# Kernel optimization log

Hardware: AMD Instinct MI355X
Metric: run time of the kernel (lower is better)

## Reference

```python
import jax, jax.numpy as jnp
import numpy as np

N = 100000   # nodes
E = 1600000  # edges (avg degree 16)
DIN = 64
DOUT = 64
EPS = 1e-12  # F.normalize eps


def setup_inputs() -> dict:
    key = jax.random.key(0)
    ks = jax.random.split(key, 10)
    x = jax.random.normal(ks[0], (N, DIN), dtype=jnp.float32)
    edge_index = jax.random.randint(ks[1], (2, E), 0, N, dtype=jnp.int32)
    edge_feature = jax.random.normal(ks[2], (E, 8), dtype=jnp.float32)
    s_in = 1.0 / np.sqrt(DIN)
    s_out = 1.0 / np.sqrt(DOUT)
    # layer 1: SAGEConv(DIN, DOUT, aggr='sum'): lin_l (bias) on aggregate, lin_r (no bias) on root
    W1l = jax.random.uniform(ks[3], (DOUT, DIN), jnp.float32, -s_in, s_in)
    b1l = jax.random.uniform(ks[4], (DOUT,), jnp.float32, -s_in, s_in)
    W1r = jax.random.uniform(ks[5], (DOUT, DIN), jnp.float32, -s_in, s_in)
    # layer 2: SAGEConv(DOUT, DOUT, aggr='sum')
    W2l = jax.random.uniform(ks[6], (DOUT, DOUT), jnp.float32, -s_out, s_out)
    b2l = jax.random.uniform(ks[7], (DOUT,), jnp.float32, -s_out, s_out)
    W2r = jax.random.uniform(ks[8], (DOUT, DOUT), jnp.float32, -s_out, s_out)
    return {"x": x, "edge_index": edge_index, "edge_feature": edge_feature,
            "W1l": W1l, "b1l": b1l, "W1r": W1r,
            "W2l": W2l, "b2l": b2l, "W2r": W2r}


def _sage_conv(x, src, dst, Wl, bl, Wr):
    # sum-aggregate neighbor messages x[src] at destination nodes
    agg = jax.ops.segment_sum(x[src], dst, num_segments=N)  # [N, d]
    return agg @ Wl.T + bl + x @ Wr.T


def reference(x, edge_index, edge_feature, W1l, b1l, W1r, W2l, b2l, W2r):
    # edge_feature is accepted by the original forward but unused
    src, dst = edge_index[0], edge_index[1]
    h = _sage_conv(x, src, dst, W1l, b1l, W1r)
    h = jax.nn.relu(h)
    nrm = jnp.linalg.norm(h, axis=-1, keepdims=True)
    h = h / jnp.maximum(nrm, EPS)  # F.normalize(dim=-1)
    # dropout is identity in eval mode
    out = _sage_conv(h, src, dst, W2l, b2l, W2r)
    return out
```

## Files before the change

kernel.cpp:

```cpp
#include <hip/hip_runtime.h>

#define NNODES 100000
#define NEDGES 1600000
#define D 64
#define EPSN 1e-12f
#define NBUK ((NNODES + 255) >> 8)
#define EPB 2048
#define LCAP 28
#define BUKCAP 4608

typedef __attribute__((ext_vector_type(8))) short short8v;
typedef __attribute__((ext_vector_type(4))) float f32x4;
typedef unsigned short ushort_t;

__device__ __forceinline__ unsigned f2bf(float f) {
    unsigned u = __float_as_uint(f);
    u = (u + 0x7FFFu + ((u >> 16) & 1u)) >> 16;
    return u;
}

__global__ __launch_bounds__(256) void cvt_bf16_kernel(
    const float* __restrict__ xin, ushort_t* __restrict__ xb)
{
    const int idx = blockIdx.x * 256 + threadIdx.x;
    if ((size_t)idx * 4 >= (size_t)NNODES * D) return;
    const float4 v = *reinterpret_cast<const float4*>(&xin[(size_t)idx * 4]);
    uint2 o;
    o.x = f2bf(v.x) | (f2bf(v.y) << 16);
    o.y = f2bf(v.z) | (f2bf(v.w) << 16);
    *reinterpret_cast<uint2*>(&xb[(size_t)idx * 4]) = o;
}

__global__ __launch_bounds__(256) void bin_scatter_kernel(
    const int* __restrict__ src,
    const int* __restrict__ dst,
    int* __restrict__ bukcnt,
    int* __restrict__ ebuf)
{
    __shared__ int lcnt[NBUK];
    __shared__ int bins[NBUK * LCAP];
    const int t = threadIdx.x;
    for (int i = t; i < NBUK; i += 256) lcnt[i] = 0;
    __syncthreads();

    const long long e0 = (long long)blockIdx.x * EPB + (long long)t * 8;
    if (e0 + 8 <= NEDGES) {
        const int4 sa = *reinterpret_cast<const int4*>(&src[e0]);
        const int4 sb = *reinterpret_cast<const int4*>(&src[e0 + 4]);
        const int4 da = *reinterpret_cast<const int4*>(&dst[e0]);
        const int4 db = *reinterpret_cast<const int4*>(&dst[e0 + 4]);
        const int dd[8] = {da.x, da.y, da.z, da.w, db.x, db.y, db.z, db.w};
        const int ss[8] = {sa.x, sa.y, sa.z, sa.w, sb.x, sb.y, sb.z, sb.w};
        #pragma unroll
        for (int i = 0; i < 8; ++i) {
            const int b = dd[i] >> 8;
            const int p = atomicAdd(&lcnt[b], 1);
            if (p < LCAP) bins[b * LCAP + p] = (ss[i] << 8) | (dd[i] & 255);
        }
    } else {
        for (long long e = e0; e < NEDGES; ++e) {
            const int d = dst[e];
            const int b = d >> 8;
            const int p = atomicAdd(&lcnt[b], 1);
            if (p < LCAP) bins[b * LCAP + p] = (src[e] << 8) | (d & 255);
        }
    }
    __syncthreads();

    for (int b = t; b < NBUK; b += 256) {
        const int cnt = min(lcnt[b], LCAP);
        if (cnt == 0) continue;
        const int base = atomicAdd(&bukcnt[b], cnt);
        for (int i = 0; i < cnt; ++i) {
            const int p = base + i;
            if (p < BUKCAP) ebuf[(size_t)b * BUKCAP + p] = bins[b * LCAP + i];
        }
    }
}

__global__ void bukscan_kernel(const int* __restrict__ bukcnt,
                               int* __restrict__ bukstart) {
    __shared__ int s[512];
    const int t = threadIdx.x;
    const int v = (t < NBUK) ? min(bukcnt[t], BUKCAP) : 0;
    int val = v;
    s[t] = val;
    __syncthreads();
    for (int off = 1; off < 512; off <<= 1) {
        int add = (t >= off) ? s[t - off] : 0;
        __syncthreads();
        val += add;
        s[t] = val;
        __syncthreads();
    }
    if (t < NBUK) bukstart[t] = val - v;
}

__global__ __launch_bounds__(256) void bucket_place_kernel(
    const int* __restrict__ bukcnt,
    const int* __restrict__ bukstart,
    const int* __restrict__ ebuf,
    int* __restrict__ rowptr,
    int* __restrict__ ssrc)
{
    __shared__ int lcnt[256];
    __shared__ int lcur[256];
    __shared__ int stmp[256];
    const int b = blockIdx.x;
    const int t = threadIdx.x;
    lcnt[t] = 0;
    lcur[t] = 0;
    __syncthreads();

    const int cnt  = min(bukcnt[b], BUKCAP);
    const int base = bukstart[b];
    const int* eb  = ebuf + (size_t)b * BUKCAP;

    for (int i = t; i < cnt; i += 256) atomicAdd(&lcnt[eb[i] & 255], 1);
    __syncthreads();

    const int v = lcnt[t];
    int val = v;
    stmp[t] = val;
    __syncthreads();
    for (int off = 1; off < 256; off <<= 1) {
        int add = (t >= off) ? stmp[t - off] : 0;
        __syncthreads();
        val += add;
        stmp[t] = val;
        __syncthreads();
    }
    const int myoff = val - v;
    __syncthreads();
    lcnt[t] = myoff;
    const int node = b * 256 + t;
    if (node < NNODES) rowptr[node] = base + myoff;
    if (b == NBUK - 1 && t == 0) rowptr[NNODES] = base + cnt;
    __syncthreads();

    for (int i = t; i < cnt; i += 256) {
        const int pv = eb[i];
        const int d = pv & 255;
        const int p = atomicAdd(&lcur[d], 1);
        ssrc[base + lcnt[d] + p] = pv >> 8;
    }
}

__global__ __launch_bounds__(256) void gather_bf16_kernel(
    const ushort_t* __restrict__ featb,
    const int* __restrict__ rowptr,
    const int* __restrict__ ssrc,
    ushort_t* __restrict__ aggb)
{
    const int tid = threadIdx.x;
    const int quarter = tid >> 4;
    const int f = tid & 15;
    const int node = blockIdx.x * 16 + quarter;
    if (node >= NNODES) return;

    const int beg = rowptr[node];
    const int end = rowptr[node + 1];
    const ushort_t* fb = featb + (size_t)f * 4;

    float ax = 0.f, ay = 0.f, az = 0.f, aw = 0.f;
    int j = beg;
    for (; j + 4 <= end; j += 4) {
        const int s0 = ssrc[j + 0];
        const int s1 = ssrc[j + 1];
        const int s2 = ssrc[j + 2];
        const int s3 = ssrc[j + 3];
        const uint2 v0 = *reinterpret_cast<const uint2*>(&fb[(size_t)s0 * D]);
        const uint2 v1 = *reinterpret_cast<const uint2*>(&fb[(size_t)s1 * D]);
        const uint2 v2 = *reinterpret_cast<const uint2*>(&fb[(size_t)s2 * D]);
        const uint2 v3 = *reinterpret_cast<const uint2*>(&fb[(size_t)s3 * D]);
        ax += __uint_as_float(v0.x << 16) + __uint_as_float(v1.x << 16)
            + __uint_as_float(v2.x << 16) + __uint_as_float(v3.x << 16);
        ay += __uint_as_float(v0.x & 0xFFFF0000u) + __uint_as_float(v1.x & 0xFFFF0000u)
            + __uint_as_float(v2.x & 0xFFFF0000u) + __uint_as_float(v3.x & 0xFFFF0000u);
        az += __uint_as_float(v0.y << 16) + __uint_as_float(v1.y << 16)
            + __uint_as_float(v2.y << 16) + __uint_as_float(v3.y << 16);
        aw += __uint_as_float(v0.y & 0xFFFF0000u) + __uint_as_float(v1.y & 0xFFFF0000u)
            + __uint_as_float(v2.y & 0xFFFF0000u) + __uint_as_float(v3.y & 0xFFFF0000u);
    }
    for (; j < end; ++j) {
        const uint2 v = *reinterpret_cast<const uint2*>(&fb[(size_t)ssrc[j] * D]);
        ax += __uint_as_float(v.x << 16);
        ay += __uint_as_float(v.x & 0xFFFF0000u);
        az += __uint_as_float(v.y << 16);
        aw += __uint_as_float(v.y & 0xFFFF0000u);
    }
    uint2 o;
    o.x = f2bf(ax) | (f2bf(ay) << 16);
    o.y = f2bf(az) | (f2bf(aw) << 16);
    *reinterpret_cast<uint2*>(&aggb[(size_t)node * D + f * 4]) = o;
}

__global__ void wprep_kernel(const float* __restrict__ W1l,
                             const float* __restrict__ W1r,
                             const float* __restrict__ W2l,
                             const float* __restrict__ W2r,
                             ushort_t* __restrict__ wfrag)
{
    const int idx = blockIdx.x * 256 + threadIdx.x;
    if (idx >= 16384) return;
    const int layer = idx >> 13;
    const int f     = (idx >> 9) & 15;
    const int lane  = (idx >> 3) & 63;
    const int b     = idx & 7;
    const int jt = f >> 2, kt = f & 3;
    const int o = jt * 16 + (lane & 15);
    const int k = kt * 32 + (lane >> 4) * 8 + b;
    const float* Wl = layer ? W2l : W1l;
    const float* Wr = layer ? W2r : W1r;
    const float v = (k < 64) ? Wl[o * 64 + k] : Wr[o * 64 + (k - 64)];
    wfrag[idx] = (ushort_t)f2bf(v);
}

#define LB(i) const short8v B##i = \
    *reinterpret_cast<const short8v*>(&wfragL[((i) * 64 + lane) * 8]);

template <bool RELU_NORM, bool BF16_OUT>
__global__ __launch_bounds__(256) void transform_mfma_kernel(
    const ushort_t* __restrict__ aggb,
    const ushort_t* __restrict__ xinb,
    const ushort_t* __restrict__ wfragL,
    const float* __restrict__ bl,
    float* __restrict__ outf,
    ushort_t* __restrict__ outb)
{
    const int tid  = threadIdx.x;
    const int w    = tid >> 6;
    const int lane = tid & 63;
    const int m    = lane & 15;
    const int kg   = lane >> 4;

    LB(0)  LB(1)  LB(2)  LB(3)  LB(4)  LB(5)  LB(6)  LB(7)
    LB(8)  LB(9)  LB(10) LB(11) LB(12) LB(13) LB(14) LB(15)

    const float bias0 = bl[m];
    const float bias1 = bl[16 + m];
    const float bias2 = bl[32 + m];
    const float bias3 = bl[48 + m];

    const int ngroups = NNODES / 16;
    for (int g = blockIdx.x * 4 + w; g < ngroups; g += gridDim.x * 4) {
        const size_t rb = (size_t)(g * 16 + m) * D;
        const short8v A0 = *reinterpret_cast<const short8v*>(&aggb[rb + kg * 8]);
        const short8v A1 = *reinterpret_cast<const short8v*>(&aggb[rb + 32 + kg * 8]);
        const short8v A2 = *reinterpret_cast<const short8v*>(&xinb[rb + kg * 8]);
        const short8v A3 = *reinterpret_cast<const short8v*>(&xinb[rb + 32 + kg * 8]);

        f32x4 acc0 = {0.f, 0.f, 0.f, 0.f};
        f32x4 acc1 = acc0, acc2 = acc0, acc3 = acc0;
        acc0 = __builtin_amdgcn_mfma_f32_16x16x32_bf16(A0, B0,  acc0, 0, 0, 0);
        acc0 = __builtin_amdgcn_mfma_f32_16x16x32_bf16(A1, B1,  acc0, 0, 0, 0);
        acc0 = __builtin_amdgcn_mfma_f32_16x16x32_bf16(A2, B2,  acc0, 0, 0, 0);
        acc0 = __builtin_amdgcn_mfma_f32_16x16x32_bf16(A3, B3,  acc0, 0, 0, 0);
        acc1 = __builtin_amdgcn_mfma_f32_16x16x32_bf16(A0, B4,  acc1, 0, 0, 0);
        acc1 = __builtin_amdgcn_mfma_f32_16x16x32_bf16(A1, B5,  acc1, 0, 0, 0);
        acc1 = __builtin_amdgcn_mfma_f32_16x16x32_bf16(A2, B6,  acc1, 0, 0, 0);
        acc1 = __builtin_amdgcn_mfma_f32_16x16x32_bf16(A3, B7,  acc1, 0, 0, 0);
        acc2 = __builtin_amdgcn_mfma_f32_16x16x32_bf16(A0, B8,  acc2, 0, 0, 0);
        acc2 = __builtin_amdgcn_mfma_f32_16x16x32_bf16(A1, B9,  acc2, 0, 0, 0);
        acc2 = __builtin_amdgcn_mfma_f32_16x16x32_bf16(A2, B10, acc2, 0, 0, 0);
        acc2 = __builtin_amdgcn_mfma_f32_16x16x32_bf16(A3, B11, acc2, 0, 0, 0);
        acc3 = __builtin_amdgcn_mfma_f32_16x16x32_bf16(A0, B12, acc3, 0, 0, 0);
        acc3 = __builtin_amdgcn_mfma_f32_16x16x32_bf16(A1, B13, acc3, 0, 0, 0);
        acc3 = __builtin_amdgcn_mfma_f32_16x16x32_bf16(A2, B14, acc3, 0, 0, 0);
        acc3 = __builtin_amdgcn_mfma_f32_16x16x32_bf16(A3, B15, acc3, 0, 0, 0);

        acc0 += bias0; acc1 += bias1; acc2 += bias2; acc3 += bias3;

        if (RELU_NORM) {
            #pragma unroll
            for (int r = 0; r < 4; ++r) {
                acc0[r] = fmaxf(acc0[r], 0.f);
                acc1[r] = fmaxf(acc1[r], 0.f);
                acc2[r] = fmaxf(acc2[r], 0.f);
                acc3[r] = fmaxf(acc3[r], 0.f);
            }
            float s0 = acc0[0]*acc0[0] + acc1[0]*acc1[0] + acc2[0]*acc2[0] + acc3[0]*acc3[0];
            float s1 = acc0[1]*acc0[1] + acc1[1]*acc1[1] + acc2[1]*acc2[1] + acc3[1]*acc3[1];
            float s2 = acc0[2]*acc0[2] + acc1[2]*acc1[2] + acc2[2]*acc2[2] + acc3[2]*acc3[2];
            float s3 = acc0[3]*acc0[3] + acc1[3]*acc1[3] + acc2[3]*acc2[3] + acc3[3]*acc3[3];
            #pragma unroll
            for (int mm = 1; mm < 16; mm <<= 1) {
                s0 += __shfl_xor(s0, mm, 64);
                s1 += __shfl_xor(s1, mm, 64);
                s2 += __shfl_xor(s2, mm, 64);
                s3 += __shfl_xor(s3, mm, 64);
            }
            const float i0 = 1.f / fmaxf(sqrtf(s0), EPSN);
            const float i1 = 1.f / fmaxf(sqrtf(s1), EPSN);
            const float i2 = 1.f / fmaxf(sqrtf(s2), EPSN);
            const float i3 = 1.f / fmaxf(sqrtf(s3), EPSN);
            acc0[0] *= i0; acc1[0] *= i0; acc2[0] *= i0; acc3[0] *= i0;
            acc0[1] *= i1; acc1[1] *= i1; acc2[1] *= i1; acc3[1] *= i1;
            acc0[2] *= i2; acc1[2] *= i2; acc2[2] *= i2; acc3[2] *= i2;
            acc0[3] *= i3; acc1[3] *= i3; acc2[3] *= i3; acc3[3] *= i3;
        }

        #pragma unroll
        for (int r = 0; r < 4; ++r) {
            const size_t row = (size_t)(g * 16 + kg * 4 + r) * D + m;
            if (BF16_OUT) {
                outb[row]      = (ushort_t)f2bf(acc0[r]);
                outb[row + 16] = (ushort_t)f2bf(acc1[r]);
                outb[row + 32] = (ushort_t)f2bf(acc2[r]);
                outb[row + 48] = (ushort_t)f2bf(acc3[r]);
            } else {
                outf[row]      = acc0[r];
                outf[row + 16] = acc1[r];
                outf[row + 32] = acc2[r];
                outf[row + 48] = acc3[r];
            }
        }
    }
}

extern "C" void kernel_launch(void* const* d_in, const int* in_sizes, int n_in,
                              void* d_out, int out_size, void* d_ws, size_t ws_size,
                              hipStream_t stream) {
    const float* x   = (const float*)d_in[0];
    const int* eidx  = (const int*)d_in[1];
    const float* W1l = (const float*)d_in[3];
    const float* b1l = (const float*)d_in[4];
    const float* W1r = (const float*)d_in[5];
    const float* W2l = (const float*)d_in[6];
    const float* b2l = (const float*)d_in[7];
    const float* W2r = (const float*)d_in[8];
    float* out = (float*)d_out;

    const int* src = eidx;
    const int* dst = eidx + NEDGES;

    char* ws = (char*)d_ws;
    int* bukcnt   = (int*)ws;  ws += ((size_t)NBUK * 4 + 15) / 16 * 16;
    int* bukstart = (int*)ws;  ws += ((size_t)NBUK * 4 + 15) / 16 * 16;
    int* rowptr   = (int*)ws;  ws += ((size_t)(NNODES + 1) * 4 + 15) / 16 * 16;
    int* ssrc     = (int*)ws;  ws += ((size_t)NEDGES * 4 + 15) / 16 * 16;
    ushort_t* wfrag = (ushort_t*)ws;  ws += ((size_t)16384 * 2 + 15) / 16 * 16;
    ushort_t* xb  = (ushort_t*)ws;    ws += (size_t)NNODES * D * 2;
    ushort_t* hb  = (ushort_t*)ws;    ws += (size_t)NNODES * D * 2;
    ushort_t* aggb = (ushort_t*)ws;   ws += (size_t)NNODES * D * 2;
    int* ebuf = (int*)aggb;

    dim3 blk(256);
    dim3 bgrid((NEDGES + EPB - 1) / EPB);
    dim3 cgrid(((NNODES * D / 4) + 255) / 256);
    dim3 ggrid((NNODES + 15) / 16);
    dim3 tgrid(1024);

    hipMemsetAsync(bukcnt, 0, (size_t)NBUK * 4, stream);
    cvt_bf16_kernel<<<cgrid, blk, 0, stream>>>(x, xb);
    wprep_kernel<<<64, blk, 0, stream>>>(W1l, W1r, W2l, W2r, wfrag);
    bin_scatter_kernel<<<bgrid, blk, 0, stream>>>(src, dst, bukcnt, ebuf);
    bukscan_kernel<<<1, 512, 0, stream>>>(bukcnt, bukstart);
    bucket_place_kernel<<<NBUK, blk, 0, stream>>>(bukcnt, bukstart, ebuf,
                                                  rowptr, ssrc);

    gather_bf16_kernel<<<ggrid, blk, 0, stream>>>(xb, rowptr, ssrc, aggb);
    transform_mfma_kernel<true, true><<<tgrid, blk, 0, stream>>>(
        aggb, xb, wfrag, b1l, nullptr, hb);

    gather_bf16_kernel<<<ggrid, blk, 0, stream>>>(hb, rowptr, ssrc, aggb);
    transform_mfma_kernel<false, false><<<tgrid, blk, 0, stream>>>(
        aggb, hb, wfrag + 8192, b2l, out, nullptr);
}
```

Measured before the change: 187.9 us.

## Split bf16 features into four planar slices and gather each slice separately

Node features are stored as four planes of 16 bf16 columns each, and each gather becomes four passes that each touch a 3.2 MB plane. The aim is to let each plane's random-access working set fit in L2/LLC so neighbour gathers hit cache more often. The costs are four times as many index reads and kernel launches, 32-byte row reads instead of 128-byte ones, and scattered 2-byte stores in the planar output of the transform.

```diff
diff --git a/kernel.cpp b/kernel.cpp
--- a/kernel.cpp
+++ b/kernel.cpp
@@ -8,10 +8,12 @@
 #define EPB 2048
 #define LCAP 28
 #define BUKCAP 4608
+#define PL ((size_t)NNODES * 16)
 
 typedef __attribute__((ext_vector_type(8))) short short8v;
 typedef __attribute__((ext_vector_type(4))) float f32x4;
 typedef unsigned short ushort_t;
+typedef unsigned int uint_t;
 
 __device__ __forceinline__ unsigned f2bf(float f) {
     unsigned u = __float_as_uint(f);
@@ -19,16 +21,22 @@
     return u;
 }
 
-__global__ __launch_bounds__(256) void cvt_bf16_kernel(
-    const float* __restrict__ xin, ushort_t* __restrict__ xb)
+__global__ __launch_bounds__(256) void cvt_planar_kernel(
+    const float* __restrict__ xin, ushort_t* __restrict__ xbP)
 {
     const int idx = blockIdx.x * 256 + threadIdx.x;
-    if ((size_t)idx * 4 >= (size_t)NNODES * D) return;
-    const float4 v = *reinterpret_cast<const float4*>(&xin[(size_t)idx * 4]);
-    uint2 o;
-    o.x = f2bf(v.x) | (f2bf(v.y) << 16);
-    o.y = f2bf(v.z) | (f2bf(v.w) << 16);
-    *reinterpret_cast<uint2*>(&xb[(size_t)idx * 4]) = o;
+    if (idx >= NNODES * 8) return;
+    const int node = idx >> 3;
+    const int oct  = idx & 7;
+    const float4 a = *reinterpret_cast<const float4*>(&xin[(size_t)node * D + oct * 8]);
+    const float4 b = *reinterpret_cast<const float4*>(&xin[(size_t)node * D + oct * 8 + 4]);
+    uint4 o;
+    o.x = f2bf(a.x) | (f2bf(a.y) << 16);
+    o.y = f2bf(a.z) | (f2bf(a.w) << 16);
+    o.z = f2bf(b.x) | (f2bf(b.y) << 16);
+    o.w = f2bf(b.z) | (f2bf(b.w) << 16);
+    ushort_t* dst = xbP + (size_t)(oct >> 1) * PL + (size_t)node * 16 + (oct & 1) * 8;
+    *reinterpret_cast<uint4*>(dst) = o;
 }
 
 __global__ __launch_bounds__(256) void bin_scatter_kernel(
@@ -146,53 +154,45 @@
     }
 }
 
-__global__ __launch_bounds__(256) void gather_bf16_kernel(
-    const ushort_t* __restrict__ featb,
+__global__ __launch_bounds__(256) void gather_pass_kernel(
+    const ushort_t* __restrict__ featP,
     const int* __restrict__ rowptr,
     const int* __restrict__ ssrc,
-    ushort_t* __restrict__ aggb)
-{
-    const int tid = threadIdx.x;
-    const int quarter = tid >> 4;
-    const int f = tid & 15;
-    const int node = blockIdx.x * 16 + quarter;
+    ushort_t* __restrict__ aggP)
+{
+    const int tid  = threadIdx.x;
+    const int grp  = tid >> 3;
+    const int l    = tid & 7;
+    const int node = blockIdx.x * 32 + grp;
     if (node >= NNODES) return;
 
     const int beg = rowptr[node];
     const int end = rowptr[node + 1];
-    const ushort_t* fb = featb + (size_t)f * 4;
-
-    float ax = 0.f, ay = 0.f, az = 0.f, aw = 0.f;
+    const ushort_t* fb = featP + l * 2;
+
+    float ax = 0.f, ay = 0.f;
     int j = beg;
     for (; j + 4 <= end; j += 4) {
         const int s0 = ssrc[j + 0];
         const int s1 = ssrc[j + 1];
         const int s2 = ssrc[j + 2];
         const int s3 = ssrc[j + 3];
-        const uint2 v0 = *reinterpret_cast<const uint2*>(&fb[(size_t)s0 * D]);
-        const uint2 v1 = *reinterpret_cast<const uint2*>(&fb[(size_t)s1 * D]);
-        const uint2 v2 = *reinterpret_cast<const uint2*>(&fb[(size_t)s2 * D]);
-        const uint2 v3 = *reinterpret_cast<const uint2*>(&fb[(size_t)s3 * D]);
-        ax += __uint_as_float(v0.x << 16) + __uint_as_float(v1.x << 16)
-            + __uint_as_float(v2.x << 16) + __uint_as_float(v3.x << 16);
-        ay += __uint_as_float(v0.x & 0xFFFF0000u) + __uint_as_float(v1.x & 0xFFFF0000u)
-            + __uint_as_float(v2.x & 0xFFFF0000u) + __uint_as_float(v3.x & 0xFFFF0000u);
-        az += __uint_as_float(v0.y << 16) + __uint_as_float(v1.y << 16)
-            + __uint_as_float(v2.y << 16) + __uint_as_float(v3.y << 16);
-        aw += __uint_as_float(v0.y & 0xFFFF0000u) + __uint_as_float(v1.y & 0xFFFF0000u)
-            + __uint_as_float(v2.y & 0xFFFF0000u) + __uint_as_float(v3.y & 0xFFFF0000u);
+        const uint_t v0 = *reinterpret_cast<const uint_t*>(&fb[(size_t)s0 * 16]);
+        const uint_t v1 = *reinterpret_cast<const uint_t*>(&fb[(size_t)s1 * 16]);
+        const uint_t v2 = *reinterpret_cast<const uint_t*>(&fb[(size_t)s2 * 16]);
+        const uint_t v3 = *reinterpret_cast<const uint_t*>(&fb[(size_t)s3 * 16]);
+        ax += __uint_as_float(v0 << 16) + __uint_as_float(v1 << 16)
+            + __uint_as_float(v2 << 16) + __uint_as_float(v3 << 16);
+        ay += __uint_as_float(v0 & 0xFFFF0000u) + __uint_as_float(v1 & 0xFFFF0000u)
+            + __uint_as_float(v2 & 0xFFFF0000u) + __uint_as_float(v3 & 0xFFFF0000u);
     }
     for (; j < end; ++j) {
-        const uint2 v = *reinterpret_cast<const uint2*>(&fb[(size_t)ssrc[j] * D]);
-        ax += __uint_as_float(v.x << 16);
-        ay += __uint_as_float(v.x & 0xFFFF0000u);
-        az += __uint_as_float(v.y << 16);
-        aw += __uint_as_float(v.y & 0xFFFF0000u);
-    }
-    uint2 o;
-    o.x = f2bf(ax) | (f2bf(ay) << 16);
-    o.y = f2bf(az) | (f2bf(aw) << 16);
-    *reinterpret_cast<uint2*>(&aggb[(size_t)node * D + f * 4]) = o;
+        const uint_t v = *reinterpret_cast<const uint_t*>(&fb[(size_t)ssrc[j] * 16]);
+        ax += __uint_as_float(v << 16);
+        ay += __uint_as_float(v & 0xFFFF0000u);
+    }
+    *reinterpret_cast<uint_t*>(&aggP[(size_t)node * 16 + l * 2]) =
+        f2bf(ax) | (f2bf(ay) << 16);
 }
 
 __global__ void wprep_kernel(const float* __restrict__ W1l,
@@ -221,12 +221,12 @@
 
 template <bool RELU_NORM, bool BF16_OUT>
 __global__ __launch_bounds__(256) void transform_mfma_kernel(
-    const ushort_t* __restrict__ aggb,
-    const ushort_t* __restrict__ xinb,
+    const ushort_t* __restrict__ aggP,
+    const ushort_t* __restrict__ xinP,
     const ushort_t* __restrict__ wfragL,
     const float* __restrict__ bl,
     float* __restrict__ outf,
-    ushort_t* __restrict__ outb)
+    ushort_t* __restrict__ outbP)
 {
     const int tid  = threadIdx.x;
     const int w    = tid >> 6;
@@ -242,13 +242,15 @@
     const float bias2 = bl[32 + m];
     const float bias3 = bl[48 + m];
 
+    const size_t poff = (size_t)(kg >> 1) * PL + (size_t)(kg & 1) * 8;
+
     const int ngroups = NNODES / 16;
     for (int g = blockIdx.x * 4 + w; g < ngroups; g += gridDim.x * 4) {
-        const size_t rb = (size_t)(g * 16 + m) * D;
-        const short8v A0 = *reinterpret_cast<const short8v*>(&aggb[rb + kg * 8]);
-        const short8v A1 = *reinterpret_cast<const short8v*>(&aggb[rb + 32 + kg * 8]);
-        const short8v A2 = *reinterpret_cast<const short8v*>(&xinb[rb + kg * 8]);
-        const short8v A3 = *reinterpret_cast<const short8v*>(&xinb[rb + 32 + kg * 8]);
+        const size_t row16 = (size_t)(g * 16 + m) * 16;
+        const short8v A0 = *reinterpret_cast<const short8v*>(&aggP[poff + row16]);
+        const short8v A1 = *reinterpret_cast<const short8v*>(&aggP[poff + 2 * PL + row16]);
+        const short8v A2 = *reinterpret_cast<const short8v*>(&xinP[poff + row16]);
+        const short8v A3 = *reinterpret_cast<const short8v*>(&xinP[poff + 2 * PL + row16]);
 
         f32x4 acc0 = {0.f, 0.f, 0.f, 0.f};
         f32x4 acc1 = acc0, acc2 = acc0, acc3 = acc0;
@@ -302,13 +304,15 @@
 
         #pragma unroll
         for (int r = 0; r < 4; ++r) {
-            const size_t row = (size_t)(g * 16 + kg * 4 + r) * D + m;
+            const int nrow = g * 16 + kg * 4 + r;
             if (BF16_OUT) {
-                outb[row]      = (ushort_t)f2bf(acc0[r]);
-                outb[row + 16] = (ushort_t)f2bf(acc1[r]);
-                outb[row + 32] = (ushort_t)f2bf(acc2[r]);
-                outb[row + 48] = (ushort_t)f2bf(acc3[r]);
+                const size_t rb16 = (size_t)nrow * 16 + m;
+                outbP[rb16]          = (ushort_t)f2bf(acc0[r]);
+                outbP[PL + rb16]     = (ushort_t)f2bf(acc1[r]);
+                outbP[2 * PL + rb16] = (ushort_t)f2bf(acc2[r]);
+                outbP[3 * PL + rb16] = (ushort_t)f2bf(acc3[r]);
             } else {
+                const size_t row = (size_t)nrow * D + m;
                 outf[row]      = acc0[r];
                 outf[row + 16] = acc1[r];
                 outf[row + 32] = acc2[r];
@@ -340,30 +344,34 @@
     int* rowptr   = (int*)ws;  ws += ((size_t)(NNODES + 1) * 4 + 15) / 16 * 16;
     int* ssrc     = (int*)ws;  ws += ((size_t)NEDGES * 4 + 15) / 16 * 16;
     ushort_t* wfrag = (ushort_t*)ws;  ws += ((size_t)16384 * 2 + 15) / 16 * 16;
-    ushort_t* xb  = (ushort_t*)ws;    ws += (size_t)NNODES * D * 2;
-    ushort_t* hb  = (ushort_t*)ws;    ws += (size_t)NNODES * D * 2;
-    ushort_t* aggb = (ushort_t*)ws;   ws += (size_t)NNODES * D * 2;
-    int* ebuf = (int*)aggb;
+    ushort_t* xbP  = (ushort_t*)ws;   ws += PL * 4 * 2;
+    ushort_t* hbP  = (ushort_t*)ws;   ws += PL * 4 * 2;
+    ushort_t* aggP = (ushort_t*)ws;   ws += PL * 4 * 2;
+    int* ebuf = (int*)aggP;
 
     dim3 blk(256);
     dim3 bgrid((NEDGES + EPB - 1) / EPB);
-    dim3 cgrid(((NNODES * D / 4) + 255) / 256);
-    dim3 ggrid((NNODES + 15) / 16);
+    dim3 cgrid((NNODES * 8 + 255) / 256);
+    dim3 pgrid((NNODES + 31) / 32);
     dim3 tgrid(1024);
 
     hipMemsetAsync(bukcnt, 0, (size_t)NBUK * 4, stream);
-    cvt_bf16_kernel<<<cgrid, blk, 0, stream>>>(x, xb);
+    cvt_planar_kernel<<<cgrid, blk, 0, stream>>>(x, xbP);
     wprep_kernel<<<64, blk, 0, stream>>>(W1l, W1r, W2l, W2r, wfrag);
     bin_scatter_kernel<<<bgrid, blk, 0, stream>>>(src, dst, bukcnt, ebuf);
     bukscan_kernel<<<1, 512, 0, stream>>>(bukcnt, bukstart);
     bucket_place_kernel<<<NBUK, blk, 0, stream>>>(bukcnt, bukstart, ebuf,
                                                   rowptr, ssrc);
 
-    gather_bf16_kernel<<<ggrid, blk, 0, stream>>>(xb, rowptr, ssrc, aggb);
+    for (int p = 0; p < 4; ++p)
+        gather_pass_kernel<<<pgrid, blk, 0, stream>>>(
+            xbP + (size_t)p * PL, rowptr, ssrc, aggP + (size_t)p * PL);
     transform_mfma_kernel<true, true><<<tgrid, blk, 0, stream>>>(
-        aggb, xb, wfrag, b1l, nullptr, hb);
-
-    gather_bf16_kernel<<<ggrid, blk, 0, stream>>>(hb, rowptr, ssrc, aggb);
+        aggP, xbP, wfrag, b1l, nullptr, hbP);
+
+    for (int p = 0; p < 4; ++p)
+        gather_pass_kernel<<<pgrid, blk, 0, stream>>>(
+            hbP + (size_t)p * PL, rowptr, ssrc, aggP + (size_t)p * PL);
     transform_mfma_kernel<false, false><<<tgrid, blk, 0, stream>>>(
-        aggb, hb, wfrag + 8192, b2l, out, nullptr);
-}
+        aggP, hbP, wfrag + 8192, b2l, out, nullptr);
+}
```

Result: slower. 232.7 us (+23.8%).

## Fuse neighbor gather with MFMA transform per 16-node block

Applied to the files above, without the earlier changes.

Merges the gather kernel and the MFMA transform kernel into one kernel per layer. Each 16-node block aggregates neighbor rows into shared memory, loads the root features, and each wave computes one 16-column output slice with MFMA, adding a cross-wave shared-memory reduction for the L2 normalization. This removes the intermediate aggregate buffer round trip through global memory and two launches. In exchange each wave now reloads its weight fragments per block, adds __syncthreads barriers, and ebuf gets its own workspace region because it can no longer alias the removed aggregate buffer.

```diff
diff --git a/kernel.cpp b/kernel.cpp
--- a/kernel.cpp
+++ b/kernel.cpp
@@ -146,17 +146,57 @@
     }
 }
 
-__global__ __launch_bounds__(256) void gather_bf16_kernel(
+__global__ void wprep_kernel(const float* __restrict__ W1l,
+                             const float* __restrict__ W1r,
+                             const float* __restrict__ W2l,
+                             const float* __restrict__ W2r,
+                             ushort_t* __restrict__ wfrag)
+{
+    const int idx = blockIdx.x * 256 + threadIdx.x;
+    if (idx >= 16384) return;
+    const int layer = idx >> 13;
+    const int f     = (idx >> 9) & 15;
+    const int lane  = (idx >> 3) & 63;
+    const int b     = idx & 7;
+    const int jt = f >> 2, kt = f & 3;
+    const int o = jt * 16 + (lane & 15);
+    const int k = kt * 32 + (lane >> 4) * 8 + b;
+    const float* Wl = layer ? W2l : W1l;
+    const float* Wr = layer ? W2r : W1r;
+    const float v = (k < 64) ? Wl[o * 64 + k] : Wr[o * 64 + (k - 64)];
+    wfrag[idx] = (ushort_t)f2bf(v);
+}
+
+template <bool RELU_NORM, bool BF16_OUT>
+__global__ __launch_bounds__(256) void sage_gather_mfma_kernel(
     const ushort_t* __restrict__ featb,
     const int* __restrict__ rowptr,
     const int* __restrict__ ssrc,
-    ushort_t* __restrict__ aggb)
-{
+    const ushort_t* __restrict__ wfragL,
+    const float* __restrict__ bl,
+    float* __restrict__ outf,
+    ushort_t* __restrict__ outb)
+{
+    __shared__ ushort_t at[16][72];
+    __shared__ ushort_t xt[16][72];
+    __shared__ float ssq[4][16];
+
     const int tid = threadIdx.x;
     const int quarter = tid >> 4;
     const int f = tid & 15;
-    const int node = blockIdx.x * 16 + quarter;
-    if (node >= NNODES) return;
+    const int node0 = blockIdx.x * 16;
+    const int node = node0 + quarter;
+
+    const int w    = tid >> 6;
+    const int lane = tid & 63;
+    const int m    = lane & 15;
+    const int kg   = lane >> 4;
+
+    const short8v Bw0 = *reinterpret_cast<const short8v*>(&wfragL[((w * 4 + 0) * 64 + lane) * 8]);
+    const short8v Bw1 = *reinterpret_cast<const short8v*>(&wfragL[((w * 4 + 1) * 64 + lane) * 8]);
+    const short8v Bw2 = *reinterpret_cast<const short8v*>(&wfragL[((w * 4 + 2) * 64 + lane) * 8]);
+    const short8v Bw3 = *reinterpret_cast<const short8v*>(&wfragL[((w * 4 + 3) * 64 + lane) * 8]);
+    const float bias = bl[w * 16 + m];
 
     const int beg = rowptr[node];
     const int end = rowptr[node + 1];
@@ -189,132 +229,61 @@
         az += __uint_as_float(v.y << 16);
         aw += __uint_as_float(v.y & 0xFFFF0000u);
     }
-    uint2 o;
-    o.x = f2bf(ax) | (f2bf(ay) << 16);
-    o.y = f2bf(az) | (f2bf(aw) << 16);
-    *reinterpret_cast<uint2*>(&aggb[(size_t)node * D + f * 4]) = o;
-}
-
-__global__ void wprep_kernel(const float* __restrict__ W1l,
-                             const float* __restrict__ W1r,
-                             const float* __restrict__ W2l,
-                             const float* __restrict__ W2r,
-                             ushort_t* __restrict__ wfrag)
-{
-    const int idx = blockIdx.x * 256 + threadIdx.x;
-    if (idx >= 16384) return;
-    const int layer = idx >> 13;
-    const int f     = (idx >> 9) & 15;
-    const int lane  = (idx >> 3) & 63;
-    const int b     = idx & 7;
-    const int jt = f >> 2, kt = f & 3;
-    const int o = jt * 16 + (lane & 15);
-    const int k = kt * 32 + (lane >> 4) * 8 + b;
-    const float* Wl = layer ? W2l : W1l;
-    const float* Wr = layer ? W2r : W1r;
-    const float v = (k < 64) ? Wl[o * 64 + k] : Wr[o * 64 + (k - 64)];
-    wfrag[idx] = (ushort_t)f2bf(v);
-}
-
-#define LB(i) const short8v B##i = \
-    *reinterpret_cast<const short8v*>(&wfragL[((i) * 64 + lane) * 8]);
-
-template <bool RELU_NORM, bool BF16_OUT>
-__global__ __launch_bounds__(256) void transform_mfma_kernel(
-    const ushort_t* __restrict__ aggb,
-    const ushort_t* __restrict__ xinb,
-    const ushort_t* __restrict__ wfragL,
-    const float* __restrict__ bl,
-    float* __restrict__ outf,
-    ushort_t* __restrict__ outb)
-{
-    const int tid  = threadIdx.x;
-    const int w    = tid >> 6;
-    const int lane = tid & 63;
-    const int m    = lane & 15;
-    const int kg   = lane >> 4;
-
-    LB(0)  LB(1)  LB(2)  LB(3)  LB(4)  LB(5)  LB(6)  LB(7)
-    LB(8)  LB(9)  LB(10) LB(11) LB(12) LB(13) LB(14) LB(15)
-
-    const float bias0 = bl[m];
-    const float bias1 = bl[16 + m];
-    const float bias2 = bl[32 + m];
-    const float bias3 = bl[48 + m];
-
-    const int ngroups = NNODES / 16;
-    for (int g = blockIdx.x * 4 + w; g < ngroups; g += gridDim.x * 4) {
-        const size_t rb = (size_t)(g * 16 + m) * D;
-        const short8v A0 = *reinterpret_cast<const short8v*>(&aggb[rb + kg * 8]);
-        const short8v A1 = *reinterpret_cast<const short8v*>(&aggb[rb + 32 + kg * 8]);
-        const short8v A2 = *reinterpret_cast<const short8v*>(&xinb[rb + kg * 8]);
-        const short8v A3 = *reinterpret_cast<const short8v*>(&xinb[rb + 32 + kg * 8]);
-
-        f32x4 acc0 = {0.f, 0.f, 0.f, 0.f};
-        f32x4 acc1 = acc0, acc2 = acc0, acc3 = acc0;
-        acc0 = __builtin_amdgcn_mfma_f32_16x16x32_bf16(A0, B0,  acc0, 0, 0, 0);
-        acc0 = __builtin_amdgcn_mfma_f32_16x16x32_bf16(A1, B1,  acc0, 0, 0, 0);
-        acc0 = __builtin_amdgcn_mfma_f32_16x16x32_bf16(A2, B2,  acc0, 0, 0, 0);
-        acc0 = __builtin_amdgcn_mfma_f32_16x16x32_bf16(A3, B3,  acc0, 0, 0, 0);
-        acc1 = __builtin_amdgcn_mfma_f32_16x16x32_bf16(A0, B4,  acc1, 0, 0, 0);
-        acc1 = __builtin_amdgcn_mfma_f32_16x16x32_bf16(A1, B5,  acc1, 0, 0, 0);
-        acc1 = __builtin_amdgcn_mfma_f32_16x16x32_bf16(A2, B6,  acc1, 0, 0, 0);
-        acc1 = __builtin_amdgcn_mfma_f32_16x16x32_bf16(A3, B7,  acc1, 0, 0, 0);
-        acc2 = __builtin_amdgcn_mfma_f32_16x16x32_bf16(A0, B8,  acc2, 0, 0, 0);
-        acc2 = __builtin_amdgcn_mfma_f32_16x16x32_bf16(A1, B9,  acc2, 0, 0, 0);
-        acc2 = __builtin_amdgcn_mfma_f32_16x16x32_bf16(A2, B10, acc2, 0, 0, 0);
-        acc2 = __builtin_amdgcn_mfma_f32_16x16x32_bf16(A3, B11, acc2, 0, 0, 0);
-        acc3 = __builtin_amdgcn_mfma_f32_16x16x32_bf16(A0, B12, acc3, 0, 0, 0);
-        acc3 = __builtin_amdgcn_mfma_f32_16x16x32_bf16(A1, B13, acc3, 0, 0, 0);
-        acc3 = __builtin_amdgcn_mfma_f32_16x16x32_bf16(A2, B14, acc3, 0, 0, 0);
-        acc3 = __builtin_amdgcn_mfma_f32_16x16x32_bf16(A3, B15, acc3, 0, 0, 0);
-
-        acc0 += bias0; acc1 += bias1; acc2 += bias2; acc3 += bias3;
-
-        if (RELU_NORM) {
-            #pragma unroll
-            for (int r = 0; r < 4; ++r) {
-                acc0[r] = fmaxf(acc0[r], 0.f);
-                acc1[r] = fmaxf(acc1[r], 0.f);
-                acc2[r] = fmaxf(acc2[r], 0.f);
-                acc3[r] = fmaxf(acc3[r], 0.f);
-            }
-            float s0 = acc0[0]*acc0[0] + acc1[0]*acc1[0] + acc2[0]*acc2[0] + acc3[0]*acc3[0];
-            float s1 = acc0[1]*acc0[1] + acc1[1]*acc1[1] + acc2[1]*acc2[1] + acc3[1]*acc3[1];
-            float s2 = acc0[2]*acc0[2] + acc1[2]*acc1[2] + acc2[2]*acc2[2] + acc3[2]*acc3[2];
-            float s3 = acc0[3]*acc0[3] + acc1[3]*acc1[3] + acc2[3]*acc2[3] + acc3[3]*acc3[3];
-            #pragma unroll
-            for (int mm = 1; mm < 16; mm <<= 1) {
-                s0 += __shfl_xor(s0, mm, 64);
-                s1 += __shfl_xor(s1, mm, 64);
-                s2 += __shfl_xor(s2, mm, 64);
-                s3 += __shfl_xor(s3, mm, 64);
-            }
-            const float i0 = 1.f / fmaxf(sqrtf(s0), EPSN);
-            const float i1 = 1.f / fmaxf(sqrtf(s1), EPSN);
-            const float i2 = 1.f / fmaxf(sqrtf(s2), EPSN);
-            const float i3 = 1.f / fmaxf(sqrtf(s3), EPSN);
-            acc0[0] *= i0; acc1[0] *= i0; acc2[0] *= i0; acc3[0] *= i0;
-            acc0[1] *= i1; acc1[1] *= i1; acc2[1] *= i1; acc3[1] *= i1;
-            acc0[2] *= i2; acc1[2] *= i2; acc2[2] *= i2; acc3[2] *= i2;
-            acc0[3] *= i3; acc1[3] *= i3; acc2[3] *= i3; acc3[3] *= i3;
-        }
-
+    uint2 arow;
+    arow.x = f2bf(ax) | (f2bf(ay) << 16);
+    arow.y = f2bf(az) | (f2bf(aw) << 16);
+    *reinterpret_cast<uint2*>(&at[quarter][f * 4]) = arow;
+    *reinterpret_cast<uint2*>(&xt[quarter][f * 4]) =
+        *reinterpret_cast<const uint2*>(&featb[(size_t)node * D + f * 4]);
+    __syncthreads();
+
+    const short8v A0 = *reinterpret_cast<const short8v*>(&at[m][kg * 8]);
+    const short8v A1 = *reinterpret_cast<const short8v*>(&at[m][32 + kg * 8]);
+    const short8v A2 = *reinterpret_cast<const short8v*>(&xt[m][kg * 8]);
+    const short8v A3 = *reinterpret_cast<const short8v*>(&xt[m][32 + kg * 8]);
+
+    f32x4 acc = {0.f, 0.f, 0.f, 0.f};
+    acc = __builtin_amdgcn_mfma_f32_16x16x32_bf16(A0, Bw0, acc, 0, 0, 0);
+    acc = __builtin_amdgcn_mfma_f32_16x16x32_bf16(A1, Bw1, acc, 0, 0, 0);
+    acc = __builtin_amdgcn_mfma_f32_16x16x32_bf16(A2, Bw2, acc, 0, 0, 0);
+    acc = __builtin_amdgcn_mfma_f32_16x16x32_bf16(A3, Bw3, acc, 0, 0, 0);
+    acc += bias;
+
+    if (RELU_NORM) {
+        float s0, s1, s2, s3;
+        #pragma unroll
+        for (int r = 0; r < 4; ++r) acc[r] = fmaxf(acc[r], 0.f);
+        s0 = acc[0] * acc[0];
+        s1 = acc[1] * acc[1];
+        s2 = acc[2] * acc[2];
+        s3 = acc[3] * acc[3];
+        #pragma unroll
+        for (int mm = 1; mm < 16; mm <<= 1) {
+            s0 += __shfl_xor(s0, mm, 64);
+            s1 += __shfl_xor(s1, mm, 64);
+            s2 += __shfl_xor(s2, mm, 64);
+            s3 += __shfl_xor(s3, mm, 64);
+        }
+        if (m == 0) {
+            ssq[w][kg * 4 + 0] = s0;
+            ssq[w][kg * 4 + 1] = s1;
+            ssq[w][kg * 4 + 2] = s2;
+            ssq[w][kg * 4 + 3] = s3;
+        }
+        __syncthreads();
         #pragma unroll
         for (int r = 0; r < 4; ++r) {
-            const size_t row = (size_t)(g * 16 + kg * 4 + r) * D + m;
-            if (BF16_OUT) {
-                outb[row]      = (ushort_t)f2bf(acc0[r]);
-                outb[row + 16] = (ushort_t)f2bf(acc1[r]);
-                outb[row + 32] = (ushort_t)f2bf(acc2[r]);
-                outb[row + 48] = (ushort_t)f2bf(acc3[r]);
-            } else {
-                outf[row]      = acc0[r];
-                outf[row + 16] = acc1[r];
-                outf[row + 32] = acc2[r];
-                outf[row + 48] = acc3[r];
-            }
-        }
+            const int n = kg * 4 + r;
+            const float tot = ssq[0][n] + ssq[1][n] + ssq[2][n] + ssq[3][n];
+            acc[r] *= 1.f / fmaxf(sqrtf(tot), EPSN);
+        }
+    }
+
+    #pragma unroll
+    for (int r = 0; r < 4; ++r) {
+        const size_t row = (size_t)(node0 + kg * 4 + r) * D + w * 16 + m;
+        if (BF16_OUT) outb[row] = (ushort_t)f2bf(acc[r]);
+        else          outf[row] = acc[r];
     }
 }
 
@@ -342,14 +311,12 @@
     ushort_t* wfrag = (ushort_t*)ws;  ws += ((size_t)16384 * 2 + 15) / 16 * 16;
     ushort_t* xb  = (ushort_t*)ws;    ws += (size_t)NNODES * D * 2;
     ushort_t* hb  = (ushort_t*)ws;    ws += (size_t)NNODES * D * 2;
-    ushort_t* aggb = (ushort_t*)ws;   ws += (size_t)NNODES * D * 2;
-    int* ebuf = (int*)aggb;
+    int* ebuf     = (int*)ws;         ws += ((size_t)NBUK * BUKCAP * 4 + 15) / 16 * 16;
 
     dim3 blk(256);
     dim3 bgrid((NEDGES + EPB - 1) / EPB);
     dim3 cgrid(((NNODES * D / 4) + 255) / 256);
-    dim3 ggrid((NNODES + 15) / 16);
-    dim3 tgrid(1024);
+    dim3 fgrid(NNODES / 16);
 
     hipMemsetAsync(bukcnt, 0, (size_t)NBUK * 4, stream);
     cvt_bf16_kernel<<<cgrid, blk, 0, stream>>>(x, xb);
@@ -359,11 +326,9 @@
     bucket_place_kernel<<<NBUK, blk, 0, stream>>>(bukcnt, bukstart, ebuf,
                                                   rowptr, ssrc);
 
-    gather_bf16_kernel<<<ggrid, blk, 0, stream>>>(xb, rowptr, ssrc, aggb);
-    transform_mfma_kernel<true, true><<<tgrid, blk, 0, stream>>>(
-        aggb, xb, wfrag, b1l, nullptr, hb);
-
-    gather_bf16_kernel<<<ggrid, blk, 0, stream>>>(hb, rowptr, ssrc, aggb);
-    transform_mfma_kernel<false, false><<<tgrid, blk, 0, stream>>>(
-        aggb, hb, wfrag + 8192, b2l, out, nullptr);
-}
+    sage_gather_mfma_kernel<true, true><<<fgrid, blk, 0, stream>>>(
+        xb, rowptr, ssrc, wfrag, b1l, nullptr, hb);
+
+    sage_gather_mfma_kernel<false, false><<<fgrid, blk, 0, stream>>>(
+        hb, rowptr, ssrc, wfrag + 8192, b2l, out, nullptr);
+}
```

After: 176.4 us. 6.1% less time.
